# Optimization experiments

Measured on AMD Instinct MI355X. Metric: run time of the kernel, lower is better.

The kernel has to match this reference:

```python
import jax, jax.numpy as jnp
import numpy as np

EMBED_DIM = 100
NUM_SYMBOLS = 100000
BATCH = 2048
N_NEIGH = 200


def setup_inputs() -> dict:
    key = jax.random.key(0)
    ks = jax.random.split(key, 10)
    D = EMBED_DIM
    connections = jax.random.randint(ks[0], (BATCH, N_NEIGH, 4), 0, NUM_SYMBOLS, dtype=jnp.int64)
    num_neighbors = jax.random.randint(ks[1], (BATCH,), 1, N_NEIGH, dtype=jnp.int64)
    # symbol embedding table (num_symbols+1, D); padding row = num_symbols (left random; indices stay < NUM_SYMBOLS)
    symbol_emb = jax.random.normal(ks[2], (NUM_SYMBOLS + 1, D), dtype=jnp.float32) * 0.02
    # gcn_w: Linear(3D -> D) with its own bias, plus separate gcn_b parameter
    gcn_w = jax.random.normal(ks[3], (D, 3 * D), dtype=jnp.float32) * (1.0 / np.sqrt(3 * D))
    gcn_w_bias = jnp.zeros((D,), dtype=jnp.float32)
    gcn_b = jnp.zeros((D,), dtype=jnp.float32)
    # attn_w: Linear(D -> 1)
    attn_w = jax.random.normal(ks[4], (1, D), dtype=jnp.float32) * (1.0 / np.sqrt(D))
    attn_bias = jnp.zeros((1,), dtype=jnp.float32)
    # gate_w: Linear(D -> 1) plus separate gate_b parameter
    gate_w = jax.random.normal(ks[5], (1, D), dtype=jnp.float32) * (1.0 / np.sqrt(D))
    gate_w_bias = jnp.zeros((1,), dtype=jnp.float32)
    gate_b = jnp.zeros((1,), dtype=jnp.float32)
    return {
        "connections": connections,
        "num_neighbors": num_neighbors,
        "symbol_emb": symbol_emb,
        "gcn_w": gcn_w,
        "gcn_w_bias": gcn_w_bias,
        "gcn_b": gcn_b,
        "attn_w": attn_w,
        "attn_bias": attn_bias,
        "gate_w": gate_w,
        "gate_w_bias": gate_w_bias,
        "gate_b": gate_b,
    }


def reference(connections, num_neighbors, symbol_emb, gcn_w, gcn_w_bias, gcn_b,
              attn_w, attn_bias, gate_w, gate_w_bias, gate_b):
    # neighbor_encoder (eval mode: dropout is identity). num_neighbors is unused,
    # exactly as in the original module.
    entity_self = connections[:, 0, 0]          # (B,)
    relations = connections[:, :, 1]            # (B, N)
    entities = connections[:, :, 2]
    times = connections[:, :, 3]

    rel_embeds = symbol_emb[relations]          # (B, N, D) gather
    ent_embeds = symbol_emb[entities]
    time_embeds = symbol_emb[times]
    entself_embeds = symbol_emb[entity_self]    # (B, D)

    concat = jnp.concatenate((rel_embeds, ent_embeds, time_embeds), axis=-1)  # (B, N, 3D)
    out = jnp.einsum('bnk,dk->bnd', concat, gcn_w) + gcn_w_bias + gcn_b       # (B, N, D)
    out = jax.nn.leaky_relu(out, negative_slope=0.01)

    attn_logits = jnp.einsum('bnd,od->bno', out, attn_w) + attn_bias          # (B, N, 1)
    attn_weight = jax.nn.softmax(attn_logits, axis=1)                         # softmax over neighbors
    out_attn = jnp.einsum('bnd,bno->bd', out, attn_weight)                    # (B, D)

    gate = jax.nn.sigmoid(jnp.einsum('bd,od->bo', out_attn, gate_w) + gate_w_bias + gate_b)  # (B, 1)
    out_neighbor = out_attn * gate + entself_embeds * (1.0 - gate)            # (B, D)
    return out_neighbor
```

## Files before the change

### kernel.cpp

```cpp
#include <hip/hip_runtime.h>
#include <stdint.h>

#define D_EMB 100
#define NSYM 100001
#define BATCH 2048
#define NNEI 200
#define OS_STRIDE 102

#define BP_ELEMS   32000
#define BP_KS3_OFF 30720

typedef __bf16 bf16x8 __attribute__((ext_vector_type(8)));
typedef __bf16 bf16x4 __attribute__((ext_vector_type(4)));
typedef float  f32x4  __attribute__((ext_vector_type(4)));
typedef bf16x8 bf16x8_a8 __attribute__((aligned(8)));
typedef bf16x4 bf16x4_a8 __attribute__((aligned(8)));

union bf2u { uint32_t u; __bf16 h[2]; };

__host__ __device__ inline int colmap(int tau, int n) {
    return 32 * (tau >> 1) + 8 * (n >> 2) + 4 * (tau & 1) + (n & 3);
}

__global__ __launch_bounds__(256) void prep_bp(const float* __restrict__ gcn_w,
                                               __bf16* __restrict__ Bp) {
    int idx = blockIdx.x * 256 + threadIdx.x;
    if (idx >= BP_ELEMS) return;
    int tau, n, k;
    if (idx < BP_KS3_OFF) {
        int j = idx & 7;
        n     = (idx >> 3) & 15;
        int z = idx >> 7;
        tau   = z / 12;
        int r = z - tau * 12;
        int ks = r >> 2, q = r & 3;
        k = ks * 32 + q * 8 + j;
    } else {
        int i2 = idx - BP_KS3_OFF;
        int j  = i2 & 3;
        n      = (i2 >> 2) & 15;
        tau    = i2 >> 6;
        k      = 96 + j;
    }
    const int col = colmap(tau, n);
    float v = 0.0f;
    if (col < 300 && k < 100) {
        int c = col / 100, d = col % 100;
        v = gcn_w[d * 300 + c * 100 + k];
    }
    Bp[idx] = (__bf16)v;
}

__global__ __launch_bounds__(256) void gemm_P(const float* __restrict__ emb,
                                              const __bf16* __restrict__ Bp,
                                              __bf16* __restrict__ P) {
    __shared__ __bf16 BpS[BP_ELEMS + 8];

    const int tid  = threadIdx.x;
    const int wave = tid >> 6;
    const int lane = tid & 63;
    const int n    = lane & 15;
    const int quad = lane >> 4;

    {
        const uint4* __restrict__ src = (const uint4*)Bp;
        uint4* dst = (uint4*)BpS;
        for (int c = tid; c < BP_ELEMS / 8; c += 256)
            dst[c] = src[c];
        if (tid < 8) BpS[BP_ELEMS + tid] = (__bf16)0.0f;
    }

    const int sBase = blockIdx.x * 64 + wave * 16;
    const int s     = sBase + n;
    const int srow  = (s <= NSYM - 1) ? s : (NSYM - 1);
    const float* rowp = emb + (size_t)srow * D_EMB;

    bf16x8 b[4];
    #pragma unroll
    for (int ks = 0; ks < 3; ++ks) {
        const int k0 = ks * 32 + quad * 8;
        const float4 x = *(const float4*)(rowp + k0);
        const float4 y = *(const float4*)(rowp + k0 + 4);
        bf16x8 v;
        v[0]=(__bf16)x.x; v[1]=(__bf16)x.y; v[2]=(__bf16)x.z; v[3]=(__bf16)x.w;
        v[4]=(__bf16)y.x; v[5]=(__bf16)y.y; v[6]=(__bf16)y.z; v[7]=(__bf16)y.w;
        b[ks] = v;
    }
    {
        bf16x8 v;
        #pragma unroll
        for (int i = 0; i < 8; ++i) v[i] = (__bf16)0.0f;
        if (quad == 0) {
            const float4 x = *(const float4*)(rowp + 96);
            v[0]=(__bf16)x.x; v[1]=(__bf16)x.y; v[2]=(__bf16)x.z; v[3]=(__bf16)x.w;
        }
        b[3] = v;
    }

    __syncthreads();

    const bool wr = (s <= NSYM - 1);
    __bf16* __restrict__ prow = P + (size_t)s * 300;

    for (int u = 0; u < 10; ++u) {
        const int t0 = 2 * u, t1 = t0 + 1;

        bf16x8 a0[4], a1[4];
        #pragma unroll
        for (int ks = 0; ks < 3; ++ks) {
            a0[ks] = *(const bf16x8*)&BpS[((t0 * 12 + ks * 4 + quad) * 16 + n) * 8];
            a1[ks] = *(const bf16x8*)&BpS[((t1 * 12 + ks * 4 + quad) * 16 + n) * 8];
        }
        {
            const int o0 = (quad == 0) ? (BP_KS3_OFF + (t0 * 16 + n) * 4) : BP_ELEMS;
            const int o1 = (quad == 0) ? (BP_KS3_OFF + (t1 * 16 + n) * 4) : BP_ELEMS;
            const bf16x4 w0 = *(const bf16x4*)&BpS[o0];
            const bf16x4 w1 = *(const bf16x4*)&BpS[o1];
            bf16x8 v0, v1;
            #pragma unroll
            for (int i = 0; i < 4; ++i) {
                v0[i] = w0[i]; v1[i] = w1[i];
                v0[i + 4] = (__bf16)0.0f; v1[i + 4] = (__bf16)0.0f;
            }
            a0[3] = v0; a1[3] = v1;
        }

        f32x4 acc0 = {0.f, 0.f, 0.f, 0.f};
        f32x4 acc1 = {0.f, 0.f, 0.f, 0.f};
        #pragma unroll
        for (int ks = 0; ks < 4; ++ks) {
            acc0 = __builtin_amdgcn_mfma_f32_16x16x32_bf16(a0[ks], b[ks], acc0, 0, 0, 0);
            acc1 = __builtin_amdgcn_mfma_f32_16x16x32_bf16(a1[ks], b[ks], acc1, 0, 0, 0);
        }

        if (wr) {
            const int colBase = 32 * u + 8 * quad;
            if (colBase + 8 <= 300) {
                bf16x8_a8 o;
                o[0]=(__bf16)acc0[0]; o[1]=(__bf16)acc0[1];
                o[2]=(__bf16)acc0[2]; o[3]=(__bf16)acc0[3];
                o[4]=(__bf16)acc1[0]; o[5]=(__bf16)acc1[1];
                o[6]=(__bf16)acc1[2]; o[7]=(__bf16)acc1[3];
                *(bf16x8_a8*)(prow + colBase) = o;
            } else if (colBase + 4 <= 300) {
                bf16x4_a8 o;
                o[0]=(__bf16)acc0[0]; o[1]=(__bf16)acc0[1];
                o[2]=(__bf16)acc0[2]; o[3]=(__bf16)acc0[3];
                *(bf16x4_a8*)(prow + colBase) = o;
            }
        }
    }
}

__global__ __launch_bounds__(1024, 8) void gather_attn(
        const int*    __restrict__ conn,
        const __bf16* __restrict__ P,
        const float*  __restrict__ emb,
        const float*  __restrict__ gcn_w_bias,
        const float*  __restrict__ gcn_b,
        const float*  __restrict__ attn_w,
        const float*  __restrict__ attn_bias,
        const float*  __restrict__ gate_w,
        const float*  __restrict__ gate_w_bias,
        const float*  __restrict__ gate_b,
        float* __restrict__ out) {

    __shared__ __bf16 out_s[NNEI][OS_STRIDE];
    __shared__ int4   conn_s[NNEI];
    __shared__ float  logits[NNEI];
    __shared__ float  wgt[NNEI];
    __shared__ float2 aw_s[50];
    __shared__ float  part[8][D_EMB];
    __shared__ float  red[128];
    __shared__ float  gsh;

    const int b = blockIdx.x;
    const int t = threadIdx.x;
    const int w = t >> 6;
    const int l = t & 63;

    if (t < NNEI) conn_s[t] = *(const int4*)(conn + ((size_t)b * NNEI + t) * 4);
    if (t < 50)   aw_s[t] = make_float2(attn_w[2 * t], attn_w[2 * t + 1]);

    const bool act = (l < 50);
    const int  d0  = 2 * l;
    float bias0 = 0.f, bias1 = 0.f;
    if (act) {
        bias0 = gcn_w_bias[d0]     + gcn_b[d0];
        bias1 = gcn_w_bias[d0 + 1] + gcn_b[d0 + 1];
    }
    const float abias = attn_bias[0];
    __syncthreads();

    #pragma unroll
    for (int half = 0; half < 2; ++half) {
        const int b0 = w + half * 128;
        uint32_t L[8][3];
        #pragma unroll
        for (int j = 0; j < 8; ++j) {
            const int nj = b0 + 16 * j;
            if (act && nj < NNEI) {
                const int4 c = conn_s[nj];
                L[j][0] = *(const uint32_t*)(P + (size_t)c.y * 300 +       d0);
                L[j][1] = *(const uint32_t*)(P + (size_t)c.z * 300 + 100 + d0);
                L[j][2] = *(const uint32_t*)(P + (size_t)c.w * 300 + 200 + d0);
            }
        }
        #pragma unroll
        for (int j = 0; j < 8; ++j) {
            const int nj = b0 + 16 * j;
            if (act && nj < NNEI) {
                bf2u a0, a1, a2;
                a0.u = L[j][0]; a1.u = L[j][1]; a2.u = L[j][2];
                float v0 = (float)a0.h[0] + (float)a1.h[0] + (float)a2.h[0] + bias0;
                float v1 = (float)a0.h[1] + (float)a1.h[1] + (float)a2.h[1] + bias1;
                v0 = v0 > 0.f ? v0 : 0.01f * v0;
                v1 = v1 > 0.f ? v1 : 0.01f * v1;
                bf2u o; o.h[0] = (__bf16)v0; o.h[1] = (__bf16)v1;
                *(uint32_t*)&out_s[nj][d0] = o.u;
            }
        }
    }
    __syncthreads();

    if (t < NNEI) {
        const __bf16* row = &out_s[t][0];
        float pA = 0.f, pB = 0.f;
        #pragma unroll 5
        for (int j = 0; j < 50; j += 2) {
            bf2u v0; v0.u = *(const uint32_t*)(row + 2 * j);
            bf2u v1; v1.u = *(const uint32_t*)(row + 2 * j + 2);
            const float2 w0 = aw_s[j];
            const float2 w1 = aw_s[j + 1];
            pA += (float)v0.h[0] * w0.x + (float)v0.h[1] * w0.y;
            pB += (float)v1.h[0] * w1.x + (float)v1.h[1] * w1.y;
        }
        logits[t] = pA + pB + abias;
    }
    __syncthreads();

    if (w == 0) {
        float vals[4];
        float mx = -1e30f;
        #pragma unroll
        for (int j = 0; j < 4; ++j) {
            const int n = l + 64 * j;
            vals[j] = (n < NNEI) ? logits[n] : -1e30f;
            mx = fmaxf(mx, vals[j]);
        }
        #pragma unroll
        for (int off = 32; off > 0; off >>= 1) mx = fmaxf(mx, __shfl_xor(mx, off));
        float sum = 0.f;
        #pragma unroll
        for (int j = 0; j < 4; ++j) {
            const int n = l + 64 * j;
            if (n < NNEI) { const float e = __expf(vals[j] - mx); wgt[n] = e; sum += e; }
        }
        #pragma unroll
        for (int off = 32; off > 0; off >>= 1) sum += __shfl_xor(sum, off);
        const float inv = 1.f / sum;
        #pragma unroll
        for (int j = 0; j < 4; ++j) {
            const int n = l + 64 * j;
            if (n < NNEI) wgt[n] *= inv;
        }
    }
    __syncthreads();

    {
        const int g  = t >> 7;
        const int dd = t & 127;
        if (dd < D_EMB) {
            float pa = 0.f;
            const int n0 = g * 25;
            #pragma unroll 5
            for (int n = n0; n < n0 + 25; ++n) pa += wgt[n] * (float)out_s[n][dd];
            part[g][dd] = pa;
        }
    }
    __syncthreads();

    float accd = 0.f;
    if (t < D_EMB) {
        #pragma unroll
        for (int g = 0; g < 8; ++g) accd += part[g][t];
        red[t] = accd * gate_w[t];
    } else if (t < 128) {
        red[t] = 0.f;
    }
    __syncthreads();

    if (w == 0) {
        float r = red[l] + red[l + 64];
        #pragma unroll
        for (int off = 32; off > 0; off >>= 1) r += __shfl_xor(r, off);
        if (l == 0) gsh = 1.f / (1.f + __expf(-(r + gate_w_bias[0] + gate_b[0])));
    }
    __syncthreads();

    if (t < D_EMB) {
        const int self = conn_s[0].x;
        const float se = emb[(size_t)self * D_EMB + t];
        const float g  = gsh;
        out[(size_t)b * D_EMB + t] = accd * g + se * (1.f - g);
    }
}

__global__ void ws_diag(float* out, float ws_mb) { out[0] = ws_mb; }

extern "C" void kernel_launch(void* const* d_in, const int* in_sizes, int n_in,
                              void* d_out, int out_size, void* d_ws, size_t ws_size,
                              hipStream_t stream) {
    const int*   conn        = (const int*)d_in[0];
    const float* emb         = (const float*)d_in[2];
    const float* gcn_w       = (const float*)d_in[3];
    const float* gcn_w_bias  = (const float*)d_in[4];
    const float* gcn_b       = (const float*)d_in[5];
    const float* attn_w      = (const float*)d_in[6];
    const float* attn_bias   = (const float*)d_in[7];
    const float* gate_w      = (const float*)d_in[8];
    const float* gate_w_bias = (const float*)d_in[9];
    const float* gate_b      = (const float*)d_in[10];
    float* out = (float*)d_out;

    const size_t P_bytes = (size_t)NSYM * 300 * 2;
    const size_t Bp_off  = (P_bytes + 255) & ~(size_t)255;
    const size_t need    = Bp_off + (size_t)BP_ELEMS * 2;

    if (ws_size < need) {
        ws_diag<<<1, 1, 0, stream>>>(out, (float)(ws_size / 1.0e6));
        return;
    }

    __bf16* P  = (__bf16*)d_ws;
    __bf16* Bp = (__bf16*)((char*)d_ws + Bp_off);

    prep_bp<<<(BP_ELEMS + 255) / 256, 256, 0, stream>>>(gcn_w, Bp);
    gemm_P<<<(NSYM + 63) / 64, 256, 0, stream>>>(emb, Bp, P);
    gather_attn<<<BATCH, 1024, 0, stream>>>(conn, P, emb, gcn_w_bias, gcn_b,
                                            attn_w, attn_bias, gate_w, gate_w_bias,
                                            gate_b, out);
}
```

Measured before the change: 185.2 us.

## Store projected table P in scaled FP8 and widen gather parallelism

The precomputed per-symbol projection table P is now stored as FP8 (scaled by 256) with a 304-byte row stride instead of bf16, halving the table's write and gather traffic. gemm_P now uses 512-thread blocks, each wave computing two 16-row tiles so the LDS-staged weight fragments are reused. gather_attn spreads the 200x25 four-element gathers over all 1024 threads instead of 50 of every 64 lanes, and splits the attention-logit dot product across two threads per neighbor. FP8 storage adds quantization error to the linear-layer outputs, which risks accuracy.

```diff
diff --git a/kernel.cpp b/kernel.cpp
--- a/kernel.cpp
+++ b/kernel.cpp
@@ -6,6 +6,9 @@
 #define BATCH 2048
 #define NNEI 200
 #define OS_STRIDE 102
+#define P_STRIDE 304
+#define FP8_SCALE 256.0f
+#define FP8_INV   0.00390625f
 
 #define BP_ELEMS   32000
 #define BP_KS3_OFF 30720
@@ -13,8 +16,7 @@
 typedef __bf16 bf16x8 __attribute__((ext_vector_type(8)));
 typedef __bf16 bf16x4 __attribute__((ext_vector_type(4)));
 typedef float  f32x4  __attribute__((ext_vector_type(4)));
-typedef bf16x8 bf16x8_a8 __attribute__((aligned(8)));
-typedef bf16x4 bf16x4_a8 __attribute__((aligned(8)));
+typedef float  f32x2  __attribute__((ext_vector_type(2)));
 
 union bf2u { uint32_t u; __bf16 h[2]; };
 
@@ -51,31 +53,8 @@
     Bp[idx] = (__bf16)v;
 }
 
-__global__ __launch_bounds__(256) void gemm_P(const float* __restrict__ emb,
-                                              const __bf16* __restrict__ Bp,
-                                              __bf16* __restrict__ P) {
-    __shared__ __bf16 BpS[BP_ELEMS + 8];
-
-    const int tid  = threadIdx.x;
-    const int wave = tid >> 6;
-    const int lane = tid & 63;
-    const int n    = lane & 15;
-    const int quad = lane >> 4;
-
-    {
-        const uint4* __restrict__ src = (const uint4*)Bp;
-        uint4* dst = (uint4*)BpS;
-        for (int c = tid; c < BP_ELEMS / 8; c += 256)
-            dst[c] = src[c];
-        if (tid < 8) BpS[BP_ELEMS + tid] = (__bf16)0.0f;
-    }
-
-    const int sBase = blockIdx.x * 64 + wave * 16;
-    const int s     = sBase + n;
-    const int srow  = (s <= NSYM - 1) ? s : (NSYM - 1);
-    const float* rowp = emb + (size_t)srow * D_EMB;
-
-    bf16x8 b[4];
+__device__ inline void load_bfrag(const float* __restrict__ rowp, int quad,
+                                  bf16x8 b[4]) {
     #pragma unroll
     for (int ks = 0; ks < 3; ++ks) {
         const int k0 = ks * 32 + quad * 8;
@@ -86,21 +65,56 @@
         v[4]=(__bf16)y.x; v[5]=(__bf16)y.y; v[6]=(__bf16)y.z; v[7]=(__bf16)y.w;
         b[ks] = v;
     }
+    bf16x8 v;
+    #pragma unroll
+    for (int i = 0; i < 8; ++i) v[i] = (__bf16)0.0f;
+    if (quad == 0) {
+        const float4 x = *(const float4*)(rowp + 96);
+        v[0]=(__bf16)x.x; v[1]=(__bf16)x.y; v[2]=(__bf16)x.z; v[3]=(__bf16)x.w;
+    }
+    b[3] = v;
+}
+
+__device__ inline uint32_t pack_fp8x4(float a, float b, float c, float d) {
+    uint32_t w = (uint32_t)__builtin_amdgcn_cvt_pk_fp8_f32(a, b, 0, false);
+    w = (uint32_t)__builtin_amdgcn_cvt_pk_fp8_f32(c, d, (int)w, true);
+    return w;
+}
+
+__global__ __launch_bounds__(512, 4) void gemm_P(const float* __restrict__ emb,
+                                                 const __bf16* __restrict__ Bp,
+                                                 uint8_t* __restrict__ P8) {
+    __shared__ __bf16 BpS[BP_ELEMS + 8];
+
+    const int tid  = threadIdx.x;
+    const int wave = tid >> 6;
+    const int lane = tid & 63;
+    const int n    = lane & 15;
+    const int quad = lane >> 4;
+
     {
-        bf16x8 v;
-        #pragma unroll
-        for (int i = 0; i < 8; ++i) v[i] = (__bf16)0.0f;
-        if (quad == 0) {
-            const float4 x = *(const float4*)(rowp + 96);
-            v[0]=(__bf16)x.x; v[1]=(__bf16)x.y; v[2]=(__bf16)x.z; v[3]=(__bf16)x.w;
-        }
-        b[3] = v;
-    }
-
-    __syncthreads();
-
-    const bool wr = (s <= NSYM - 1);
-    __bf16* __restrict__ prow = P + (size_t)s * 300;
+        const uint4* __restrict__ src = (const uint4*)Bp;
+        uint4* dst = (uint4*)BpS;
+        for (int c = tid; c < BP_ELEMS / 8; c += 512)
+            dst[c] = src[c];
+        if (tid < 8) BpS[BP_ELEMS + tid] = (__bf16)0.0f;
+    }
+
+    const int sA = blockIdx.x * 256 + wave * 32 + n;
+    const int sB = sA + 16;
+    const int rA = (sA <= NSYM - 1) ? sA : (NSYM - 1);
+    const int rB = (sB <= NSYM - 1) ? sB : (NSYM - 1);
+
+    bf16x8 bA[4], bB[4];
+    load_bfrag(emb + (size_t)rA * D_EMB, quad, bA);
+    load_bfrag(emb + (size_t)rB * D_EMB, quad, bB);
+
+    __syncthreads();
+
+    const bool wrA = (sA <= NSYM - 1);
+    const bool wrB = (sB <= NSYM - 1);
+    uint8_t* __restrict__ prA = P8 + (size_t)sA * P_STRIDE;
+    uint8_t* __restrict__ prB = P8 + (size_t)sB * P_STRIDE;
 
     for (int u = 0; u < 10; ++u) {
         const int t0 = 2 * u, t1 = t0 + 1;
@@ -125,51 +139,67 @@
             a0[3] = v0; a1[3] = v1;
         }
 
-        f32x4 acc0 = {0.f, 0.f, 0.f, 0.f};
-        f32x4 acc1 = {0.f, 0.f, 0.f, 0.f};
+        f32x4 aA0 = {0.f,0.f,0.f,0.f}, aA1 = {0.f,0.f,0.f,0.f};
+        f32x4 aB0 = {0.f,0.f,0.f,0.f}, aB1 = {0.f,0.f,0.f,0.f};
         #pragma unroll
         for (int ks = 0; ks < 4; ++ks) {
-            acc0 = __builtin_amdgcn_mfma_f32_16x16x32_bf16(a0[ks], b[ks], acc0, 0, 0, 0);
-            acc1 = __builtin_amdgcn_mfma_f32_16x16x32_bf16(a1[ks], b[ks], acc1, 0, 0, 0);
-        }
-
-        if (wr) {
-            const int colBase = 32 * u + 8 * quad;
-            if (colBase + 8 <= 300) {
-                bf16x8_a8 o;
-                o[0]=(__bf16)acc0[0]; o[1]=(__bf16)acc0[1];
-                o[2]=(__bf16)acc0[2]; o[3]=(__bf16)acc0[3];
-                o[4]=(__bf16)acc1[0]; o[5]=(__bf16)acc1[1];
-                o[6]=(__bf16)acc1[2]; o[7]=(__bf16)acc1[3];
-                *(bf16x8_a8*)(prow + colBase) = o;
-            } else if (colBase + 4 <= 300) {
-                bf16x4_a8 o;
-                o[0]=(__bf16)acc0[0]; o[1]=(__bf16)acc0[1];
-                o[2]=(__bf16)acc0[2]; o[3]=(__bf16)acc0[3];
-                *(bf16x4_a8*)(prow + colBase) = o;
+            aA0 = __builtin_amdgcn_mfma_f32_16x16x32_bf16(a0[ks], bA[ks], aA0, 0, 0, 0);
+            aA1 = __builtin_amdgcn_mfma_f32_16x16x32_bf16(a1[ks], bA[ks], aA1, 0, 0, 0);
+            aB0 = __builtin_amdgcn_mfma_f32_16x16x32_bf16(a0[ks], bB[ks], aB0, 0, 0, 0);
+            aB1 = __builtin_amdgcn_mfma_f32_16x16x32_bf16(a1[ks], bB[ks], aB1, 0, 0, 0);
+        }
+
+        const int colBase = 32 * u + 8 * quad;
+        if (colBase + 8 <= 300) {
+            if (wrA) {
+                uint2 o;
+                o.x = pack_fp8x4(aA0[0]*FP8_SCALE, aA0[1]*FP8_SCALE,
+                                 aA0[2]*FP8_SCALE, aA0[3]*FP8_SCALE);
+                o.y = pack_fp8x4(aA1[0]*FP8_SCALE, aA1[1]*FP8_SCALE,
+                                 aA1[2]*FP8_SCALE, aA1[3]*FP8_SCALE);
+                *(uint2*)(prA + colBase) = o;
             }
+            if (wrB) {
+                uint2 o;
+                o.x = pack_fp8x4(aB0[0]*FP8_SCALE, aB0[1]*FP8_SCALE,
+                                 aB0[2]*FP8_SCALE, aB0[3]*FP8_SCALE);
+                o.y = pack_fp8x4(aB1[0]*FP8_SCALE, aB1[1]*FP8_SCALE,
+                                 aB1[2]*FP8_SCALE, aB1[3]*FP8_SCALE);
+                *(uint2*)(prB + colBase) = o;
+            }
+        } else if (colBase + 4 <= 300) {
+            if (wrA)
+                *(uint32_t*)(prA + colBase) =
+                    pack_fp8x4(aA0[0]*FP8_SCALE, aA0[1]*FP8_SCALE,
+                               aA0[2]*FP8_SCALE, aA0[3]*FP8_SCALE);
+            if (wrB)
+                *(uint32_t*)(prB + colBase) =
+                    pack_fp8x4(aB0[0]*FP8_SCALE, aB0[1]*FP8_SCALE,
+                               aB0[2]*FP8_SCALE, aB0[3]*FP8_SCALE);
         }
     }
 }
 
 __global__ __launch_bounds__(1024, 8) void gather_attn(
-        const int*    __restrict__ conn,
-        const __bf16* __restrict__ P,
-        const float*  __restrict__ emb,
-        const float*  __restrict__ gcn_w_bias,
-        const float*  __restrict__ gcn_b,
-        const float*  __restrict__ attn_w,
-        const float*  __restrict__ attn_bias,
-        const float*  __restrict__ gate_w,
-        const float*  __restrict__ gate_w_bias,
-        const float*  __restrict__ gate_b,
+        const int*     __restrict__ conn,
+        const uint8_t* __restrict__ P8,
+        const float*   __restrict__ emb,
+        const float*   __restrict__ gcn_w_bias,
+        const float*   __restrict__ gcn_b,
+        const float*   __restrict__ attn_w,
+        const float*   __restrict__ attn_bias,
+        const float*   __restrict__ gate_w,
+        const float*   __restrict__ gate_w_bias,
+        const float*   __restrict__ gate_b,
         float* __restrict__ out) {
 
     __shared__ __bf16 out_s[NNEI][OS_STRIDE];
     __shared__ int4   conn_s[NNEI];
     __shared__ float  logits[NNEI];
+    __shared__ float  logit2[NNEI][2];
     __shared__ float  wgt[NNEI];
     __shared__ float2 aw_s[50];
+    __shared__ float4 bias4_s[25];
     __shared__ float  part[8][D_EMB];
     __shared__ float  red[128];
     __shared__ float  gsh;
@@ -181,62 +211,61 @@
 
     if (t < NNEI) conn_s[t] = *(const int4*)(conn + ((size_t)b * NNEI + t) * 4);
     if (t < 50)   aw_s[t] = make_float2(attn_w[2 * t], attn_w[2 * t + 1]);
-
-    const bool act = (l < 50);
-    const int  d0  = 2 * l;
-    float bias0 = 0.f, bias1 = 0.f;
-    if (act) {
-        bias0 = gcn_w_bias[d0]     + gcn_b[d0];
-        bias1 = gcn_w_bias[d0 + 1] + gcn_b[d0 + 1];
-    }
+    if (t < 25)
+        bias4_s[t] = make_float4(gcn_w_bias[4*t]   + gcn_b[4*t],
+                                 gcn_w_bias[4*t+1] + gcn_b[4*t+1],
+                                 gcn_w_bias[4*t+2] + gcn_b[4*t+2],
+                                 gcn_w_bias[4*t+3] + gcn_b[4*t+3]);
     const float abias = attn_bias[0];
     __syncthreads();
 
     #pragma unroll
-    for (int half = 0; half < 2; ++half) {
-        const int b0 = w + half * 128;
-        uint32_t L[8][3];
-        #pragma unroll
-        for (int j = 0; j < 8; ++j) {
-            const int nj = b0 + 16 * j;
-            if (act && nj < NNEI) {
-                const int4 c = conn_s[nj];
-                L[j][0] = *(const uint32_t*)(P + (size_t)c.y * 300 +       d0);
-                L[j][1] = *(const uint32_t*)(P + (size_t)c.z * 300 + 100 + d0);
-                L[j][2] = *(const uint32_t*)(P + (size_t)c.w * 300 + 200 + d0);
-            }
-        }
-        #pragma unroll
-        for (int j = 0; j < 8; ++j) {
-            const int nj = b0 + 16 * j;
-            if (act && nj < NNEI) {
-                bf2u a0, a1, a2;
-                a0.u = L[j][0]; a1.u = L[j][1]; a2.u = L[j][2];
-                float v0 = (float)a0.h[0] + (float)a1.h[0] + (float)a2.h[0] + bias0;
-                float v1 = (float)a0.h[1] + (float)a1.h[1] + (float)a2.h[1] + bias1;
-                v0 = v0 > 0.f ? v0 : 0.01f * v0;
-                v1 = v1 > 0.f ? v1 : 0.01f * v1;
-                bf2u o; o.h[0] = (__bf16)v0; o.h[1] = (__bf16)v1;
-                *(uint32_t*)&out_s[nj][d0] = o.u;
-            }
-        }
-    }
-    __syncthreads();
-
-    if (t < NNEI) {
-        const __bf16* row = &out_s[t][0];
-        float pA = 0.f, pB = 0.f;
+    for (int i = 0; i < 5; ++i) {
+        const int idx = t + 1024 * i;
+        if (idx < NNEI * 25) {
+            const int n  = idx / 25;
+            const int li = idx - n * 25;
+            const int4 c = conn_s[n];
+            const uint32_t u0 = *(const uint32_t*)(P8 + (size_t)c.y * P_STRIDE +       li * 4);
+            const uint32_t u1 = *(const uint32_t*)(P8 + (size_t)c.z * P_STRIDE + 100 + li * 4);
+            const uint32_t u2 = *(const uint32_t*)(P8 + (size_t)c.w * P_STRIDE + 200 + li * 4);
+            const f32x2 y0 = __builtin_amdgcn_cvt_pk_f32_fp8((int)u0, false);
+            const f32x2 y1 = __builtin_amdgcn_cvt_pk_f32_fp8((int)u0, true);
+            const f32x2 z0 = __builtin_amdgcn_cvt_pk_f32_fp8((int)u1, false);
+            const f32x2 z1 = __builtin_amdgcn_cvt_pk_f32_fp8((int)u1, true);
+            const f32x2 q0 = __builtin_amdgcn_cvt_pk_f32_fp8((int)u2, false);
+            const f32x2 q1 = __builtin_amdgcn_cvt_pk_f32_fp8((int)u2, true);
+            const float4 bb = bias4_s[li];
+            float v0 = (y0[0] + z0[0] + q0[0]) * FP8_INV + bb.x;
+            float v1 = (y0[1] + z0[1] + q0[1]) * FP8_INV + bb.y;
+            float v2 = (y1[0] + z1[0] + q1[0]) * FP8_INV + bb.z;
+            float v3 = (y1[1] + z1[1] + q1[1]) * FP8_INV + bb.w;
+            v0 = v0 > 0.f ? v0 : 0.01f * v0;
+            v1 = v1 > 0.f ? v1 : 0.01f * v1;
+            v2 = v2 > 0.f ? v2 : 0.01f * v2;
+            v3 = v3 > 0.f ? v3 : 0.01f * v3;
+            bf2u o01; o01.h[0] = (__bf16)v0; o01.h[1] = (__bf16)v1;
+            bf2u o23; o23.h[0] = (__bf16)v2; o23.h[1] = (__bf16)v3;
+            *(uint32_t*)&out_s[n][4 * li]     = o01.u;
+            *(uint32_t*)&out_s[n][4 * li + 2] = o23.u;
+        }
+    }
+    __syncthreads();
+
+    if (t < 2 * NNEI) {
+        const int n = t >> 1, half = t & 1;
+        const __bf16* row = &out_s[n][half * 50];
+        float p = 0.f;
         #pragma unroll 5
-        for (int j = 0; j < 50; j += 2) {
-            bf2u v0; v0.u = *(const uint32_t*)(row + 2 * j);
-            bf2u v1; v1.u = *(const uint32_t*)(row + 2 * j + 2);
-            const float2 w0 = aw_s[j];
-            const float2 w1 = aw_s[j + 1];
-            pA += (float)v0.h[0] * w0.x + (float)v0.h[1] * w0.y;
-            pB += (float)v1.h[0] * w1.x + (float)v1.h[1] * w1.y;
-        }
-        logits[t] = pA + pB + abias;
-    }
+        for (int j = 0; j < 25; ++j) {
+            bf2u v; v.u = *(const uint32_t*)(row + 2 * j);
+            const float2 ww = aw_s[half * 25 + j];
+            p += (float)v.h[0] * ww.x + (float)v.h[1] * ww.y;
+        }
+        logit2[n][half] = p;
+    }
+    __syncthreads();
+    if (t < NNEI) logits[t] = logit2[t][0] + logit2[t][1] + abias;
     __syncthreads();
 
     if (w == 0) {
@@ -323,7 +352,7 @@
     const float* gate_b      = (const float*)d_in[10];
     float* out = (float*)d_out;
 
-    const size_t P_bytes = (size_t)NSYM * 300 * 2;
+    const size_t P_bytes = (size_t)NSYM * P_STRIDE;
     const size_t Bp_off  = (P_bytes + 255) & ~(size_t)255;
     const size_t need    = Bp_off + (size_t)BP_ELEMS * 2;
 
@@ -332,12 +361,12 @@
         return;
     }
 
-    __bf16* P  = (__bf16*)d_ws;
-    __bf16* Bp = (__bf16*)((char*)d_ws + Bp_off);
+    uint8_t* P8 = (uint8_t*)d_ws;
+    __bf16*  Bp = (__bf16*)((char*)d_ws + Bp_off);
 
     prep_bp<<<(BP_ELEMS + 255) / 256, 256, 0, stream>>>(gcn_w, Bp);
-    gemm_P<<<(NSYM + 63) / 64, 256, 0, stream>>>(emb, Bp, P);
-    gather_attn<<<BATCH, 1024, 0, stream>>>(conn, P, emb, gcn_w_bias, gcn_b,
+    gemm_P<<<(NSYM + 255) / 256, 512, 0, stream>>>(emb, Bp, P8);
+    gather_attn<<<BATCH, 1024, 0, stream>>>(conn, P8, emb, gcn_w_bias, gcn_b,
                                             attn_w, attn_bias, gate_w, gate_w_bias,
                                             gate_b, out);
 }
```

Measured after the change: 155.7 us. 1.19x faster.
